# Optimization experiments

Measured on AMD Instinct MI355X. Metric: run time of the kernel, lower is better.

The kernel has to match this reference:

```python
import jax, jax.numpy as jnp
import numpy as np


def _cos(a, b, eps):
    # cosine similarity along last axis, clamping each norm to >= eps (torch semantics)
    na = jnp.maximum(jnp.linalg.norm(a, axis=-1), eps)
    nb = jnp.maximum(jnp.linalg.norm(b, axis=-1), eps)
    return jnp.sum(a * b, axis=-1) / (na * nb)


def setup_inputs() -> dict:
    key = jax.random.key(0)
    k1, k2, k3 = jax.random.split(key, 3)
    S, B, D = 64, 256, 1024
    logits = jax.random.normal(k1, (S, B, D), dtype=jnp.float32)
    tgt_out = jax.random.normal(k2, (S, B, D), dtype=jnp.float32)
    tgt_padding_mask = jax.random.randint(k3, (B, S), 0, 2).astype(bool)
    return {"logits": logits, "tgt_out": tgt_out, "tgt_padding_mask": tgt_padding_mask}


def reference(logits, tgt_out, tgt_padding_mask):
    S, B, D = logits.shape
    f = logits.dtype
    valid = ~tgt_padding_mask                      # (B, S) True = real sentence
    valid_sb = valid.T                             # (S, B)
    n_valid = valid.sum().astype(f)

    # masked MSE over all unpadded elements (mean over n_valid * D elements)
    m = valid_sb[:, :, None]
    loss_mse = jnp.sum(jnp.square(logits - tgt_out) * m) / (n_valid * D)

    # CosineEmbeddingLoss with target = 1: mean over valid rows of (1 - cos)
    c = _cos(logits, tgt_out, 1e-8)                # (S, B)
    loss_cos = jnp.sum((1.0 - c) * valid_sb) / n_valid

    # consecutive-sentence cosine deltas, batch-major flattening (as original loops)
    lb = jnp.swapaxes(logits, 0, 1)                # (B, S, D)
    tb = jnp.swapaxes(tgt_out, 0, 1)
    pair_valid = valid[:, :-1] & valid[:, 1:]      # (B, S-1)
    d_l = _cos(lb[:, :-1], lb[:, 1:], 1e-6)        # (B, S-1)
    d_t = _cos(tb[:, :-1], tb[:, 1:], 1e-6)
    cnt = pair_valid.sum()
    loss_delta = jnp.sum(jnp.square(d_l - d_t) * pair_valid) / jnp.maximum(cnt, 1).astype(f)

    # delta-of-delta: finite differences between CONSECUTIVE entries of the
    # compacted (valid-only, batch-major) delta list. Compact via rank scatter.
    L = B * (S - 1)
    pvf = pair_valid.reshape(-1)
    rank = jnp.cumsum(pvf) - 1
    idx = jnp.where(pvf, rank, L)                  # invalid -> out-of-bounds, dropped

    def dd(d_flat):
        dense = jnp.zeros(L, d_flat.dtype).at[idx].set(d_flat, mode="drop")
        prev = dense[:-1]
        den = jnp.where(prev != 0, prev, jnp.asarray(1e-6, d_flat.dtype))
        return (dense[1:] - prev) / den            # (L-1,)

    dd_l = dd(d_l.reshape(-1))
    dd_t = dd(d_t.reshape(-1))
    dd_valid = jnp.arange(L - 1) < (cnt - 1)
    n_dd = jnp.maximum(cnt - 1, 1).astype(f)
    loss_dd = jnp.sum(jnp.square(dd_l - dd_t) * dd_valid) / n_dd / 100.0

    return loss_mse + loss_cos + loss_delta + loss_dd
```

## Files before the change

kernel.cpp:

```cpp
#include <hip/hip_runtime.h>

#define S_DIM 64
#define B_DIM 256
#define D_DIM 1024
#define BS (B_DIM * S_DIM)
#define LP (B_DIM * (S_DIM - 1))
#define NBP 128

__device__ __forceinline__ float dot4(float4 a, float4 b) {
  return a.x * b.x + a.y * b.y + a.z * b.z + a.w * b.w;
}

template <int CTRL>
__device__ __forceinline__ float dpp_add(float v) {
  int r = __builtin_amdgcn_update_dpp(__float_as_int(v), __float_as_int(v),
                                      CTRL, 0xF, 0xF, false);
  return v + __int_as_float(r);
}

__device__ __forceinline__ float red64_uni(float v) {
  v = dpp_add<0x128>(v);
  v = dpp_add<0x124>(v);
  v = dpp_add<0x122>(v);
  v = dpp_add<0x121>(v);
  float r = __int_as_float(__builtin_amdgcn_readlane(__float_as_int(v), 0));
  r += __int_as_float(__builtin_amdgcn_readlane(__float_as_int(v), 16));
  r += __int_as_float(__builtin_amdgcn_readlane(__float_as_int(v), 32));
  r += __int_as_float(__builtin_amdgcn_readlane(__float_as_int(v), 48));
  return r;
}

__global__ __launch_bounds__(512) void row_stats_kernel(
    const float* __restrict__ logits, const float* __restrict__ tgt,
    const unsigned char* __restrict__ mask, float* __restrict__ ws) {
  const int tid = threadIdx.x;
  const int lane = tid & 63;
  const int wv = tid >> 6;
  int bid = blockIdx.x;
  bid = (bid & 7) * 256 + (bid >> 3);
  const int b  = bid >> 3;
  const int r0 = (bid & 7) << 3;
  const int k  = wv >> 1;
  const int h  = wv & 1;
  const int s0 = r0 + (k << 1);

  float* nl2p = ws;
  float* nt2p = ws + 2 * BS;
  float* ltp  = ws + 4 * BS;
  float* ajlp = ws + 6 * BS;
  float* ajtp = ws + 8 * BS;

  uchar4 det = reinterpret_cast<const uchar4*>(mask)[lane];
  const bool isbyte = __ballot((det.y | det.z | det.w) != 0) != 0ull;
  auto mvalid = [&](int s) -> bool {
    const int idx = b * S_DIM + s;
    return mask[isbyte ? idx : (idx << 2)] == 0;
  };
  const bool v0 = mvalid(s0);
  const bool v1 = mvalid(s0 + 1);
  const bool vp = (s0 > 0) && mvalid(s0 - 1);
  const bool needP  = v0 && vp;
  const bool needP1 = v0 && v1;

  const int fo = h * 128 + lane;

  __shared__ float4 lds[8][256];

  float4 R[4], N[4], P[4];

  auto ldrow = [&](int s, float4* dst) {
    const float4* Lp = reinterpret_cast<const float4*>(
        logits + ((size_t)s * B_DIM + b) * D_DIM);
    const float4* Tp = reinterpret_cast<const float4*>(
        tgt + ((size_t)s * B_DIM + b) * D_DIM);
    dst[0] = Lp[fo];
    dst[1] = Lp[fo + 64];
    dst[2] = Tp[fo];
    dst[3] = Tp[fo + 64];
  };

  if (v0) ldrow(s0, R);
  if (v1) ldrow(s0 + 1, N);
  if (k == 0 && needP) ldrow(s0 - 1, P);

  if (v1) {
    lds[wv][lane]       = N[0];
    lds[wv][lane + 64]  = N[1];
    lds[wv][lane + 128] = N[2];
    lds[wv][lane + 192] = N[3];
  }

  float a0 = 0.f, a1 = 0.f, a2 = 0.f;
  float b0 = 0.f, b1 = 0.f, b2 = 0.f, b3 = 0.f, b4 = 0.f;
  if (v0) {
    a0 = dot4(R[0], R[0]) + dot4(R[1], R[1]);
    a1 = dot4(R[2], R[2]) + dot4(R[3], R[3]);
    a2 = dot4(R[0], R[2]) + dot4(R[1], R[3]);
  }
  if (v1) {
    b0 = dot4(N[0], N[0]) + dot4(N[1], N[1]);
    b1 = dot4(N[2], N[2]) + dot4(N[3], N[3]);
    b2 = dot4(N[0], N[2]) + dot4(N[1], N[3]);
  }
  if (needP1) {
    b3 = dot4(N[0], R[0]) + dot4(N[1], R[1]);
    b4 = dot4(N[2], R[2]) + dot4(N[3], R[3]);
  }

  __syncthreads();

  float a3 = 0.f, a4 = 0.f;
  if (needP) {
    if (k != 0) {
      P[0] = lds[wv - 2][lane];
      P[1] = lds[wv - 2][lane + 64];
      P[2] = lds[wv - 2][lane + 128];
      P[3] = lds[wv - 2][lane + 192];
    }
    a3 = dot4(R[0], P[0]) + dot4(R[1], P[1]);
    a4 = dot4(R[2], P[2]) + dot4(R[3], P[3]);
  }

  if (v0) { a0 = red64_uni(a0); a1 = red64_uni(a1); a2 = red64_uni(a2); }
  if (needP) { a3 = red64_uni(a3); a4 = red64_uni(a4); }
  if (v1) { b0 = red64_uni(b0); b1 = red64_uni(b1); b2 = red64_uni(b2); }
  if (needP1) { b3 = red64_uni(b3); b4 = red64_uni(b4); }

  if (lane == 0) {
    const int i = b * S_DIM + s0;
    if (v0) { nl2p[2 * i + h] = a0; nt2p[2 * i + h] = a1; ltp[2 * i + h] = a2; }
    if (needP) { ajlp[2 * (i - 1) + h] = a3; ajtp[2 * (i - 1) + h] = a4; }
    if (v1) {
      const int i2 = i + 1;
      nl2p[2 * i2 + h] = b0; nt2p[2 * i2 + h] = b1; ltp[2 * i2 + h] = b2;
    }
    if (needP1) { ajlp[2 * i + h] = b3; ajtp[2 * i + h] = b4; }
  }
}

__device__ __forceinline__ float ld2(const float* p, int i) {
  float2 v = reinterpret_cast<const float2*>(p)[i];
  return v.x + v.y;
}

__global__ __launch_bounds__(128) void pair_kernel(
    const unsigned char* __restrict__ mask, float* __restrict__ ws) {
  const float* nl2p = ws;
  const float* nt2p = ws + 2 * BS;
  const float* ltp  = ws + 4 * BS;
  const float* ajlp = ws + 6 * BS;
  const float* ajtp = ws + 8 * BS;
  float* partial = ws + 10 * BS;

  __shared__ unsigned long long vb[16];
  __shared__ float psum[6][2];
  __shared__ int s_flag;

  const int tid = threadIdx.x;
  const int w = tid >> 6, lane = tid & 63;

  if (tid == 0) s_flag = 0;
  __syncthreads();
  int any = 0;
  for (int i = tid; i < 1024; i += 128)
    if ((i & 3) == 1 && mask[i]) any = 1;
  if (any) s_flag = 1;
  __syncthreads();
  const bool isbyte = (s_flag != 0);

  int B0 = (blockIdx.x * 128) / 63;
  if (B0 > B_DIM - 16) B0 = B_DIM - 16;

#pragma unroll
  for (int k = 0; k < 8; ++k) {
    const int q = k * 2 + w;
    const int g2 = (B0 + q) * 64 + lane;
    bool val = mask[isbyte ? g2 : (g2 << 2)] == 0;
    unsigned long long bal = __ballot(val);
    if (lane == 0) vb[q] = bal;
  }
  __syncthreads();

  const int g = blockIdx.x * 128 + tid;

  float nv = 0.f, mse = 0.f, coss = 0.f, dsum = 0.f, ddsum = 0.f, cntf = 0.f;

  if (mask[isbyte ? g : (g << 2)] == 0) {
    float A = ld2(nl2p, g), Q = ld2(nt2p, g), Cc = ld2(ltp, g);
    nv = 1.f;
    mse = A + Q - 2.f * Cc;
    coss = 1.f - Cc / (fmaxf(sqrtf(A), 1e-8f) * fmaxf(sqrtf(Q), 1e-8f));
  }

  if (g < LP) {
    const int b = g / 63;
    const int s = g - b * 63;
    const unsigned long long pbb = vb[b - B0] & (vb[b - B0] >> 1);
    if ((pbb >> s) & 1ull) {
      const int i0 = b * S_DIM + s;
      float dl = ld2(ajlp, i0) / (fmaxf(sqrtf(ld2(nl2p, i0)), 1e-6f) *
                                  fmaxf(sqrtf(ld2(nl2p, i0 + 1)), 1e-6f));
      float dt = ld2(ajtp, i0) / (fmaxf(sqrtf(ld2(nt2p, i0)), 1e-6f) *
                                  fmaxf(sqrtf(ld2(nt2p, i0 + 1)), 1e-6f));
      float wv = dl - dt;
      dsum = wv * wv;
      cntf = 1.f;

      int bq = b, sq = -1;
      bool found = false, fellback = false;
      unsigned long long cur = pbb & (~0ull << (s + 1));
      while (true) {
        if (cur) { sq = __builtin_ctzll(cur); found = true; break; }
        ++bq;
        if (bq >= B_DIM) break;
        if (bq - B0 < 16) {
          cur = vb[bq - B0] & (vb[bq - B0] >> 1);
        } else {
          fellback = true;
          break;
        }
      }
      if (fellback) {
        while (bq < B_DIM && !found) {
          for (int s2 = 0; s2 < 63; ++s2) {
            int r0 = bq * S_DIM + s2;
            bool v1 = mask[isbyte ? r0 : (r0 << 2)] == 0;
            bool v2 = mask[isbyte ? (r0 + 1) : ((r0 + 1) << 2)] == 0;
            if (v1 && v2) { sq = s2; found = true; break; }
          }
          if (!found) ++bq;
        }
      }
      if (found) {
        const int j0 = bq * S_DIM + sq;
        float dlq = ld2(ajlp, j0) / (fmaxf(sqrtf(ld2(nl2p, j0)), 1e-6f) *
                                     fmaxf(sqrtf(ld2(nl2p, j0 + 1)), 1e-6f));
        float dtq = ld2(ajtp, j0) / (fmaxf(sqrtf(ld2(nt2p, j0)), 1e-6f) *
                                     fmaxf(sqrtf(ld2(nt2p, j0 + 1)), 1e-6f));
        float ddl = (dlq - dl) / ((dl != 0.f) ? dl : 1e-6f);
        float ddt = (dtq - dt) / ((dt != 0.f) ? dt : 1e-6f);
        float u = ddl - ddt;
        ddsum = u * u;
      }
    }
  }

  float vals[6] = {nv, mse, coss, dsum, ddsum, cntf};
#pragma unroll
  for (int k2 = 0; k2 < 6; ++k2) {
    float v = red64_uni(vals[k2]);
    if (lane == 0) psum[k2][w] = v;
  }
  __syncthreads();
  if (tid == 0) {
#pragma unroll
    for (int k2 = 0; k2 < 6; ++k2)
      partial[k2 * NBP + blockIdx.x] = psum[k2][0] + psum[k2][1];
  }
}

__global__ __launch_bounds__(128) void final_combine_kernel(
    const float* __restrict__ ws, float* __restrict__ out) {
  const float* partial = ws + 10 * BS;
  __shared__ float sm[6][2];
  const int tid = threadIdx.x, w = tid >> 6, lane = tid & 63;
#pragma unroll
  for (int k = 0; k < 6; ++k) {
    float v = red64_uni(partial[k * NBP + tid]);
    if (lane == 0) sm[k][w] = v;
  }
  __syncthreads();
  if (tid == 0) {
    float nv   = sm[0][0] + sm[0][1];
    float mse  = sm[1][0] + sm[1][1];
    float coss = sm[2][0] + sm[2][1];
    float dsum = sm[3][0] + sm[3][1];
    float ddsm = sm[4][0] + sm[4][1];
    float cnt  = sm[5][0] + sm[5][1];
    out[0] = mse / (nv * (float)D_DIM) + coss / nv +
             dsum / fmaxf(cnt, 1.f) + (ddsm / fmaxf(cnt - 1.f, 1.f)) * 0.01f;
  }
}

extern "C" void kernel_launch(void* const* d_in, const int* in_sizes, int n_in,
                              void* d_out, int out_size, void* d_ws, size_t ws_size,
                              hipStream_t stream) {
  const float* logits = (const float*)d_in[0];
  const float* tgt    = (const float*)d_in[1];
  const unsigned char* mask = (const unsigned char*)d_in[2];
  float* out = (float*)d_out;
  float* ws  = (float*)d_ws;

  row_stats_kernel<<<dim3(2048), dim3(512), 0, stream>>>(logits, tgt, mask, ws);
  pair_kernel<<<dim3(NBP), dim3(128), 0, stream>>>(mask, ws);
  final_combine_kernel<<<dim3(1), dim3(128), 0, stream>>>(ws, out);
}
```

Measured before the change: 29.05 us.

## Drop LDS row sharing, reduce only within 16 lanes, store 8 partials per row

Measured after the change: 29.38 us. About the same (+1.1%).

```diff
diff --git a/kernel.cpp b/kernel.cpp
--- a/kernel.cpp
+++ b/kernel.cpp
@@ -6,6 +6,7 @@
 #define BS (B_DIM * S_DIM)
 #define LP (B_DIM * (S_DIM - 1))
 #define NBP 128
+#define PSTR 8
 
 __device__ __forceinline__ float dot4(float4 a, float4 b) {
   return a.x * b.x + a.y * b.y + a.z * b.z + a.w * b.w;
@@ -18,11 +19,16 @@
   return v + __int_as_float(r);
 }
 
-__device__ __forceinline__ float red64_uni(float v) {
+__device__ __forceinline__ float red16(float v) {
   v = dpp_add<0x128>(v);
   v = dpp_add<0x124>(v);
   v = dpp_add<0x122>(v);
   v = dpp_add<0x121>(v);
+  return v;
+}
+
+__device__ __forceinline__ float red64_uni(float v) {
+  v = red16(v);
   float r = __int_as_float(__builtin_amdgcn_readlane(__float_as_int(v), 0));
   r += __int_as_float(__builtin_amdgcn_readlane(__float_as_int(v), 16));
   r += __int_as_float(__builtin_amdgcn_readlane(__float_as_int(v), 32));
@@ -30,25 +36,23 @@
   return r;
 }
 
-__global__ __launch_bounds__(512) void row_stats_kernel(
+__global__ __launch_bounds__(256) void row_stats_kernel(
     const float* __restrict__ logits, const float* __restrict__ tgt,
     const unsigned char* __restrict__ mask, float* __restrict__ ws) {
   const int tid = threadIdx.x;
   const int lane = tid & 63;
-  const int wv = tid >> 6;
   int bid = blockIdx.x;
-  bid = (bid & 7) * 256 + (bid >> 3);
-  const int b  = bid >> 3;
-  const int r0 = (bid & 7) << 3;
-  const int k  = wv >> 1;
-  const int h  = wv & 1;
-  const int s0 = r0 + (k << 1);
+  bid = (bid & 7) * 512 + (bid >> 3);
+  const int gw = (bid << 2) | (tid >> 6);
+  const int h  = gw & 1;
+  const int s0 = ((gw >> 1) & 31) << 1;
+  const int b  = gw >> 6;
 
   float* nl2p = ws;
-  float* nt2p = ws + 2 * BS;
-  float* ltp  = ws + 4 * BS;
-  float* ajlp = ws + 6 * BS;
-  float* ajtp = ws + 8 * BS;
+  float* nt2p = ws + 8 * BS;
+  float* ltp  = ws + 16 * BS;
+  float* ajlp = ws + 24 * BS;
+  float* ajtp = ws + 32 * BS;
 
   uchar4 det = reinterpret_cast<const uchar4*>(mask)[lane];
   const bool isbyte = __ballot((det.y | det.z | det.w) != 0) != 0ull;
@@ -64,8 +68,6 @@
 
   const int fo = h * 128 + lane;
 
-  __shared__ float4 lds[8][256];
-
   float4 R[4], N[4], P[4];
 
   auto ldrow = [&](int s, float4* dst) {
@@ -81,22 +83,19 @@
 
   if (v0) ldrow(s0, R);
   if (v1) ldrow(s0 + 1, N);
-  if (k == 0 && needP) ldrow(s0 - 1, P);
-
-  if (v1) {
-    lds[wv][lane]       = N[0];
-    lds[wv][lane + 64]  = N[1];
-    lds[wv][lane + 128] = N[2];
-    lds[wv][lane + 192] = N[3];
-  }
-
-  float a0 = 0.f, a1 = 0.f, a2 = 0.f;
+  if (needP) ldrow(s0 - 1, P);
+
+  float a0 = 0.f, a1 = 0.f, a2 = 0.f, a3 = 0.f, a4 = 0.f;
   float b0 = 0.f, b1 = 0.f, b2 = 0.f, b3 = 0.f, b4 = 0.f;
   if (v0) {
     a0 = dot4(R[0], R[0]) + dot4(R[1], R[1]);
     a1 = dot4(R[2], R[2]) + dot4(R[3], R[3]);
     a2 = dot4(R[0], R[2]) + dot4(R[1], R[3]);
   }
+  if (needP) {
+    a3 = dot4(R[0], P[0]) + dot4(R[1], P[1]);
+    a4 = dot4(R[2], P[2]) + dot4(R[3], P[3]);
+  }
   if (v1) {
     b0 = dot4(N[0], N[0]) + dot4(N[1], N[1]);
     b1 = dot4(N[2], N[2]) + dot4(N[3], N[3]);
@@ -107,50 +106,38 @@
     b4 = dot4(N[2], R[2]) + dot4(N[3], R[3]);
   }
 
-  __syncthreads();
-
-  float a3 = 0.f, a4 = 0.f;
-  if (needP) {
-    if (k != 0) {
-      P[0] = lds[wv - 2][lane];
-      P[1] = lds[wv - 2][lane + 64];
-      P[2] = lds[wv - 2][lane + 128];
-      P[3] = lds[wv - 2][lane + 192];
+  if (v0) { a0 = red16(a0); a1 = red16(a1); a2 = red16(a2); }
+  if (needP) { a3 = red16(a3); a4 = red16(a4); }
+  if (v1) { b0 = red16(b0); b1 = red16(b1); b2 = red16(b2); }
+  if (needP1) { b3 = red16(b3); b4 = red16(b4); }
+
+  if ((lane & 15) == 0) {
+    const int q = lane >> 4;
+    const int i = b * S_DIM + s0;
+    const int o = PSTR * i + h * 4 + q;
+    if (v0) { nl2p[o] = a0; nt2p[o] = a1; ltp[o] = a2; }
+    if (needP) { ajlp[o - PSTR] = a3; ajtp[o - PSTR] = a4; }
+    if (v1) {
+      nl2p[o + PSTR] = b0; nt2p[o + PSTR] = b1; ltp[o + PSTR] = b2;
     }
-    a3 = dot4(R[0], P[0]) + dot4(R[1], P[1]);
-    a4 = dot4(R[2], P[2]) + dot4(R[3], P[3]);
-  }
-
-  if (v0) { a0 = red64_uni(a0); a1 = red64_uni(a1); a2 = red64_uni(a2); }
-  if (needP) { a3 = red64_uni(a3); a4 = red64_uni(a4); }
-  if (v1) { b0 = red64_uni(b0); b1 = red64_uni(b1); b2 = red64_uni(b2); }
-  if (needP1) { b3 = red64_uni(b3); b4 = red64_uni(b4); }
-
-  if (lane == 0) {
-    const int i = b * S_DIM + s0;
-    if (v0) { nl2p[2 * i + h] = a0; nt2p[2 * i + h] = a1; ltp[2 * i + h] = a2; }
-    if (needP) { ajlp[2 * (i - 1) + h] = a3; ajtp[2 * (i - 1) + h] = a4; }
-    if (v1) {
-      const int i2 = i + 1;
-      nl2p[2 * i2 + h] = b0; nt2p[2 * i2 + h] = b1; ltp[2 * i2 + h] = b2;
-    }
-    if (needP1) { ajlp[2 * i + h] = b3; ajtp[2 * i + h] = b4; }
-  }
-}
-
-__device__ __forceinline__ float ld2(const float* p, int i) {
-  float2 v = reinterpret_cast<const float2*>(p)[i];
-  return v.x + v.y;
+    if (needP1) { ajlp[o] = b3; ajtp[o] = b4; }
+  }
+}
+
+__device__ __forceinline__ float ld8(const float* p, int i) {
+  const float4* q4 = reinterpret_cast<const float4*>(p) + 2 * i;
+  float4 x = q4[0], y = q4[1];
+  return ((x.x + x.y) + (x.z + x.w)) + ((y.x + y.y) + (y.z + y.w));
 }
 
 __global__ __launch_bounds__(128) void pair_kernel(
     const unsigned char* __restrict__ mask, float* __restrict__ ws) {
   const float* nl2p = ws;
-  const float* nt2p = ws + 2 * BS;
-  const float* ltp  = ws + 4 * BS;
-  const float* ajlp = ws + 6 * BS;
-  const float* ajtp = ws + 8 * BS;
-  float* partial = ws + 10 * BS;
+  const float* nt2p = ws + 8 * BS;
+  const float* ltp  = ws + 16 * BS;
+  const float* ajlp = ws + 24 * BS;
+  const float* ajtp = ws + 32 * BS;
+  float* partial = ws + 40 * BS;
 
   __shared__ unsigned long long vb[16];
   __shared__ float psum[6][2];
@@ -186,7 +173,7 @@
   float nv = 0.f, mse = 0.f, coss = 0.f, dsum = 0.f, ddsum = 0.f, cntf = 0.f;
 
   if (mask[isbyte ? g : (g << 2)] == 0) {
-    float A = ld2(nl2p, g), Q = ld2(nt2p, g), Cc = ld2(ltp, g);
+    float A = ld8(nl2p, g), Q = ld8(nt2p, g), Cc = ld8(ltp, g);
     nv = 1.f;
     mse = A + Q - 2.f * Cc;
     coss = 1.f - Cc / (fmaxf(sqrtf(A), 1e-8f) * fmaxf(sqrtf(Q), 1e-8f));
@@ -198,10 +185,10 @@
     const unsigned long long pbb = vb[b - B0] & (vb[b - B0] >> 1);
     if ((pbb >> s) & 1ull) {
       const int i0 = b * S_DIM + s;
-      float dl = ld2(ajlp, i0) / (fmaxf(sqrtf(ld2(nl2p, i0)), 1e-6f) *
-                                  fmaxf(sqrtf(ld2(nl2p, i0 + 1)), 1e-6f));
-      float dt = ld2(ajtp, i0) / (fmaxf(sqrtf(ld2(nt2p, i0)), 1e-6f) *
-                                  fmaxf(sqrtf(ld2(nt2p, i0 + 1)), 1e-6f));
+      float dl = ld8(ajlp, i0) / (fmaxf(sqrtf(ld8(nl2p, i0)), 1e-6f) *
+                                  fmaxf(sqrtf(ld8(nl2p, i0 + 1)), 1e-6f));
+      float dt = ld8(ajtp, i0) / (fmaxf(sqrtf(ld8(nt2p, i0)), 1e-6f) *
+                                  fmaxf(sqrtf(ld8(nt2p, i0 + 1)), 1e-6f));
       float wv = dl - dt;
       dsum = wv * wv;
       cntf = 1.f;
@@ -224,19 +211,19 @@
         while (bq < B_DIM && !found) {
           for (int s2 = 0; s2 < 63; ++s2) {
             int r0 = bq * S_DIM + s2;
-            bool v1 = mask[isbyte ? r0 : (r0 << 2)] == 0;
-            bool v2 = mask[isbyte ? (r0 + 1) : ((r0 + 1) << 2)] == 0;
-            if (v1 && v2) { sq = s2; found = true; break; }
+            bool q1 = mask[isbyte ? r0 : (r0 << 2)] == 0;
+            bool q2 = mask[isbyte ? (r0 + 1) : ((r0 + 1) << 2)] == 0;
+            if (q1 && q2) { sq = s2; found = true; break; }
           }
           if (!found) ++bq;
         }
       }
       if (found) {
         const int j0 = bq * S_DIM + sq;
-        float dlq = ld2(ajlp, j0) / (fmaxf(sqrtf(ld2(nl2p, j0)), 1e-6f) *
-                                     fmaxf(sqrtf(ld2(nl2p, j0 + 1)), 1e-6f));
-        float dtq = ld2(ajtp, j0) / (fmaxf(sqrtf(ld2(nt2p, j0)), 1e-6f) *
-                                     fmaxf(sqrtf(ld2(nt2p, j0 + 1)), 1e-6f));
+        float dlq = ld8(ajlp, j0) / (fmaxf(sqrtf(ld8(nl2p, j0)), 1e-6f) *
+                                     fmaxf(sqrtf(ld8(nl2p, j0 + 1)), 1e-6f));
+        float dtq = ld8(ajtp, j0) / (fmaxf(sqrtf(ld8(nt2p, j0)), 1e-6f) *
+                                     fmaxf(sqrtf(ld8(nt2p, j0 + 1)), 1e-6f));
         float ddl = (dlq - dl) / ((dl != 0.f) ? dl : 1e-6f);
         float ddt = (dtq - dt) / ((dt != 0.f) ? dt : 1e-6f);
         float u = ddl - ddt;
@@ -261,7 +248,7 @@
 
 __global__ __launch_bounds__(128) void final_combine_kernel(
     const float* __restrict__ ws, float* __restrict__ out) {
-  const float* partial = ws + 10 * BS;
+  const float* partial = ws + 40 * BS;
   __shared__ float sm[6][2];
   const int tid = threadIdx.x, w = tid >> 6, lane = tid & 63;
 #pragma unroll
@@ -291,7 +278,7 @@
   float* out = (float*)d_out;
   float* ws  = (float*)d_ws;
 
-  row_stats_kernel<<<dim3(2048), dim3(512), 0, stream>>>(logits, tgt, mask, ws);
+  row_stats_kernel<<<dim3(4096), dim3(256), 0, stream>>>(logits, tgt, mask, ws);
   pair_kernel<<<dim3(NBP), dim3(128), 0, stream>>>(mask, ws);
   final_combine_kernel<<<dim3(1), dim3(128), 0, stream>>>(ws, out);
 }
```
